# Kernel optimization log

Measured on AMD Instinct MI355X. Metric: run time of the kernel, lower is better.

The kernel has to match this reference:

```python
import jax, jax.numpy as jnp
import numpy as np

N = 16384  # number of paired examples
D = 1024   # encoder hidden size


def setup_inputs() -> dict:
    key = jax.random.key(0)
    kx, ky = jax.random.split(key)
    x = jax.random.normal(kx, (N, D), dtype=jnp.float32)
    y = jax.random.normal(ky, (N, D), dtype=jnp.float32)
    return {"x": x, "y": y}


def reference(x, y):
    # Original: (x @ y.T).diagonal(). The diagonal of the Gram matrix is the
    # row-wise dot product, computed directly without the O(N^2 d) GEMM.
    return jnp.einsum("nd,nd->n", x, y)
```

## Files before the change

### kernel.cpp

```cpp
#include <hip/hip_runtime.h>


#define D 1024

typedef float v4f __attribute__((ext_vector_type(4)));

__device__ __forceinline__ float dot4(v4f a, v4f b) {
    return a.x * b.x + a.y * b.y + a.z * b.z + a.w * b.w;
}

__global__ __launch_bounds__(256) void rowdot_kernel(const float* __restrict__ x,
                                                     const float* __restrict__ y,
                                                     float* __restrict__ out) {
    const int wave = threadIdx.x >> 6;
    const int lane = threadIdx.x & 63;
    const int w = blockIdx.x * 4 + wave;
    const int r0 = w * 4;

    const v4f* __restrict__ xp = (const v4f*)(x + (size_t)r0 * D);
    const v4f* __restrict__ yp = (const v4f*)(y + (size_t)r0 * D);

    v4f ax[4][4];
    v4f ay[4][4];
#pragma unroll
    for (int i = 0; i < 4; ++i) {
#pragma unroll
        for (int j = 0; j < 4; ++j) {
            ax[i][j] = xp[i * 256 + j * 64 + lane];
            ay[i][j] = yp[i * 256 + j * 64 + lane];
        }
    }

    asm volatile("" ::: "memory");

    float s0 = 0.0f, s1 = 0.0f, s2 = 0.0f, s3 = 0.0f;
#pragma unroll
    for (int j = 0; j < 4; ++j) {
        s0 += dot4(ax[0][j], ay[0][j]);
        s1 += dot4(ax[1][j], ay[1][j]);
        s2 += dot4(ax[2][j], ay[2][j]);
        s3 += dot4(ax[3][j], ay[3][j]);
    }

#pragma unroll
    for (int off = 32; off > 0; off >>= 1) {
        s0 += __shfl_down(s0, off, 64);
        s1 += __shfl_down(s1, off, 64);
        s2 += __shfl_down(s2, off, 64);
        s3 += __shfl_down(s3, off, 64);
    }

    if (lane == 0) {
        *(float4*)(out + r0) = make_float4(s0, s1, s2, s3);
    }
}

extern "C" void kernel_launch(void* const* d_in, const int* in_sizes, int n_in,
                              void* d_out, int out_size, void* d_ws, size_t ws_size,
                              hipStream_t stream) {
    const float* x = (const float*)d_in[0];
    const float* y = (const float*)d_in[1];
    float* out = (float*)d_out;
    const int N = out_size;

    rowdot_kernel<<<N / 16, 256, 0, stream>>>(x, y, out);
}
```

Measured before the change: 142.1 us.

## Double-buffer row-pair loads per wave with nontemporal loads over eight rows

Each wave now handles eight rows instead of four, working through them in pairs with two register buffers. The next pair's loads are issued before the current pair is reduced, so memory latency overlaps with compute and shuffle reductions. Loads use nontemporal hints to avoid polluting the cache. The grid is halved, which lowers the number of waves available to hide latency; register pressure stays about the same.

```diff
diff --git a/kernel.cpp b/kernel.cpp
--- a/kernel.cpp
+++ b/kernel.cpp
@@ -15,44 +15,52 @@
     const int wave = threadIdx.x >> 6;
     const int lane = threadIdx.x & 63;
     const int w = blockIdx.x * 4 + wave;
-    const int r0 = w * 4;
+    const int row0 = w * 8;
 
-    const v4f* __restrict__ xp = (const v4f*)(x + (size_t)r0 * D);
-    const v4f* __restrict__ yp = (const v4f*)(y + (size_t)r0 * D);
+    const v4f* __restrict__ xp = (const v4f*)(x + (size_t)row0 * D);
+    const v4f* __restrict__ yp = (const v4f*)(y + (size_t)row0 * D);
 
-    v4f ax[4][4];
-    v4f ay[4][4];
-#pragma unroll
-    for (int i = 0; i < 4; ++i) {
+    v4f bufA[16], bufB[16];
+
+    auto issue = [&](v4f(&buf)[16], const int r) {
 #pragma unroll
         for (int j = 0; j < 4; ++j) {
-            ax[i][j] = xp[i * 256 + j * 64 + lane];
-            ay[i][j] = yp[i * 256 + j * 64 + lane];
+            buf[j]      = __builtin_nontemporal_load(&xp[(2 * r) * 256 + j * 64 + lane]);
+            buf[4 + j]  = __builtin_nontemporal_load(&yp[(2 * r) * 256 + j * 64 + lane]);
+            buf[8 + j]  = __builtin_nontemporal_load(&xp[(2 * r + 1) * 256 + j * 64 + lane]);
+            buf[12 + j] = __builtin_nontemporal_load(&yp[(2 * r + 1) * 256 + j * 64 + lane]);
         }
-    }
+    };
 
+    auto consume = [&](v4f(&buf)[16], const int r) {
+        float s0 = 0.0f, s1 = 0.0f;
+#pragma unroll
+        for (int j = 0; j < 4; ++j) {
+            s0 += dot4(buf[j], buf[4 + j]);
+            s1 += dot4(buf[8 + j], buf[12 + j]);
+        }
+#pragma unroll
+        for (int off = 32; off > 0; off >>= 1) {
+            s0 += __shfl_down(s0, off, 64);
+            s1 += __shfl_down(s1, off, 64);
+        }
+        if (lane == 0) {
+            *(float2*)(out + row0 + 2 * r) = make_float2(s0, s1);
+        }
+    };
+
+    issue(bufA, 0);
     asm volatile("" ::: "memory");
-
-    float s0 = 0.0f, s1 = 0.0f, s2 = 0.0f, s3 = 0.0f;
-#pragma unroll
-    for (int j = 0; j < 4; ++j) {
-        s0 += dot4(ax[0][j], ay[0][j]);
-        s1 += dot4(ax[1][j], ay[1][j]);
-        s2 += dot4(ax[2][j], ay[2][j]);
-        s3 += dot4(ax[3][j], ay[3][j]);
-    }
-
-#pragma unroll
-    for (int off = 32; off > 0; off >>= 1) {
-        s0 += __shfl_down(s0, off, 64);
-        s1 += __shfl_down(s1, off, 64);
-        s2 += __shfl_down(s2, off, 64);
-        s3 += __shfl_down(s3, off, 64);
-    }
-
-    if (lane == 0) {
-        *(float4*)(out + r0) = make_float4(s0, s1, s2, s3);
-    }
+    issue(bufB, 1);
+    asm volatile("" ::: "memory");
+    consume(bufA, 0);
+    issue(bufA, 2);
+    asm volatile("" ::: "memory");
+    consume(bufB, 1);
+    issue(bufB, 3);
+    asm volatile("" ::: "memory");
+    consume(bufA, 2);
+    consume(bufB, 3);
 }
 
 extern "C" void kernel_launch(void* const* d_in, const int* in_sizes, int n_in,
@@ -63,5 +71,5 @@
     float* out = (float*)d_out;
     const int N = out_size;
 
-    rowdot_kernel<<<N / 16, 256, 0, stream>>>(x, y, out);
+    rowdot_kernel<<<N / 32, 256, 0, stream>>>(x, y, out);
 }
```

Result: faster. 136.0 us (-4.3%).
